# Optimization experiments

Measured on AMD Instinct MI355X. Metric: run time of the kernel, lower is better.

Reference implementation:

```python
import jax, jax.numpy as jnp
import numpy as np

N_NODES = 50000
N_EDGES = 600000
D_IN = 128
H = 128
D_OUT = 1


def setup_inputs() -> dict:
    key = jax.random.key(0)
    ks = jax.random.split(key, 6)
    x = jax.random.normal(ks[0], (N_NODES, D_IN), dtype=jnp.float32)
    edge_index = jax.random.randint(ks[1], (2, N_EDGES), 0, N_NODES, dtype=jnp.int32)
    # Glorot-ish init for GCN weights
    W1 = jax.random.normal(ks[2], (D_IN, H), dtype=jnp.float32) / np.sqrt(D_IN)
    W2 = jax.random.normal(ks[3], (H, H), dtype=jnp.float32) / np.sqrt(H)
    W3 = jax.random.normal(ks[4], (H, D_OUT), dtype=jnp.float32) / np.sqrt(H)
    b1 = jnp.zeros((H,), jnp.float32)
    b2 = jnp.zeros((H,), jnp.float32)
    b3 = jnp.zeros((D_OUT,), jnp.float32)
    return {"x": x, "edge_index": edge_index, "W1": W1, "b1": b1,
            "W2": W2, "b2": b2, "W3": W3, "b3": b3}


def _gcn_layer(h, src, dst, norm, self_norm, W, b, n_nodes):
    # GCNConv: h' = D^{-1/2}(A+I)D^{-1/2} (h W) + b
    hw = h @ W                                        # [N, F_out]
    msg = hw[src] * norm[:, None]                     # [E, F_out] edge gather
    agg = jax.ops.segment_sum(msg, dst, num_segments=n_nodes)
    agg = agg + hw * self_norm[:, None]               # self-loop contribution
    return agg + b


def reference(x, edge_index, W1, b1, W2, b2, W3, b3):
    # NOTE: F.dropout treated as identity (deterministic eval reference).
    n = x.shape[0]
    src, dst = edge_index[0], edge_index[1]
    # symmetric normalization with self-loops (PyG gcn_norm, edge_weight=1)
    deg = jnp.zeros((n,), x.dtype).at[dst].add(1.0) + 1.0
    dis = jax.lax.rsqrt(deg)                          # deg^{-1/2}
    norm = dis[src] * dis[dst]                        # per-edge norm
    self_norm = dis * dis
    h = jax.nn.relu(_gcn_layer(x, src, dst, norm, self_norm, W1, b1, n))
    h = jax.nn.relu(_gcn_layer(h, src, dst, norm, self_norm, W2, b2, n))
    h = jax.nn.relu(_gcn_layer(h, src, dst, norm, self_norm, W3, b3, n))
    return h
```

## Files before the change

kernel.cpp:

```cpp
#include <hip/hip_runtime.h>
#include <hip/hip_fp16.h>


typedef _Float16 v8h __attribute__((ext_vector_type(8)));
typedef float v4f __attribute__((ext_vector_type(4)));

__global__ __launch_bounds__(256) void k_count_wcast(const int* __restrict__ dst,
                                                     int* __restrict__ cnt, int nE,
                                                     int BE,
                                                     const float* __restrict__ W1,
                                                     const float* __restrict__ W2,
                                                     __half* __restrict__ Wt1,
                                                     __half* __restrict__ Wt2) {
    int b = blockIdx.x;
    if (b < BE) {
        int e = b * 256 + threadIdx.x;
        if (e < nE) atomicAdd(&cnt[dst[e]], 1);
    } else {
        int i = (b - BE) * 256 + threadIdx.x;
        int k = i >> 7, c = i & 127;
        Wt1[c * 128 + k] = __float2half(W1[i]);
        Wt2[c * 128 + k] = __float2half(W2[i]);
    }
}

__global__ __launch_bounds__(256) void k_scan_blk(const int* __restrict__ cnt,
                                                  float* __restrict__ dis,
                                                  int* __restrict__ excl,
                                                  int* __restrict__ blk_sum, int nN) {
    __shared__ int sm[256];
    const int t = threadIdx.x;
    int i = blockIdx.x * 256 + t;
    int v = (i < nN) ? cnt[i] : 0;
    if (i < nN) dis[i] = rsqrtf((float)v + 1.0f);
    sm[t] = v;
    __syncthreads();
#pragma unroll
    for (int off = 1; off < 256; off <<= 1) {
        int x = (t >= off) ? sm[t - off] : 0;
        __syncthreads();
        sm[t] += x;
        __syncthreads();
    }
    if (i < nN) excl[i] = sm[t] - v;
    if (t == 255) blk_sum[blockIdx.x] = sm[255];
}

__global__ __launch_bounds__(256) void k_scan_top(int* __restrict__ blk_sum, int nB) {
    __shared__ int sm[256];
    const int t = threadIdx.x;
    int v = (t < nB) ? blk_sum[t] : 0;
    sm[t] = v;
    __syncthreads();
#pragma unroll
    for (int off = 1; off < 256; off <<= 1) {
        int x = (t >= off) ? sm[t - off] : 0;
        __syncthreads();
        sm[t] += x;
        __syncthreads();
    }
    if (t < nB) blk_sum[t] = sm[t] - v;
    if (t == 0) blk_sum[nB] = sm[255];
}

__global__ __launch_bounds__(256) void k_scan_add(const int* __restrict__ excl,
                                                  const int* __restrict__ blk_sum,
                                                  int* __restrict__ row_ptr,
                                                  int* __restrict__ cursor,
                                                  int nN, int nB) {
    int i = blockIdx.x * 256 + threadIdx.x;
    if (i < nN) {
        int v = excl[i] + blk_sum[i >> 8];
        row_ptr[i] = v;
        cursor[i] = v;
    }
    if (i == 0) row_ptr[nN] = blk_sum[nB];
}

__global__ __launch_bounds__(256) void k_bin(const int* __restrict__ src,
                                             const int* __restrict__ dst,
                                             int* __restrict__ cursor,
                                             int* __restrict__ src_csr, int nE) {
    int e = blockIdx.x * 256 + threadIdx.x;
    if (e >= nE) return;
    int s = src[e], d = dst[e];
    int pos = atomicAdd(&cursor[d], 1);
    src_csr[pos] = s;
}

__device__ __forceinline__ float4 gather_row(const float2* __restrict__ Hv,
                                             const int* __restrict__ row_ptr,
                                             const int* __restrict__ src_csr,
                                             int g, int f4) {
    int beg = row_ptr[g], end = row_ptr[g + 1];
    float2 r0 = Hv[(size_t)g * 32 + f4];
    float2 lo = __half22float2(*(__half2*)&r0.x);
    float2 hi = __half22float2(*(__half2*)&r0.y);
    float4 acc = make_float4(lo.x, lo.y, hi.x, hi.y);
    int e = beg;
    for (; e + 8 <= end; e += 8) {
        int s[8];
#pragma unroll
        for (int j = 0; j < 8; ++j) s[j] = src_csr[e + j];
        float2 r[8];
#pragma unroll
        for (int j = 0; j < 8; ++j) r[j] = Hv[(size_t)s[j] * 32 + f4];
#pragma unroll
        for (int j = 0; j < 8; ++j) {
            float2 l2 = __half22float2(*(__half2*)&r[j].x);
            float2 h2 = __half22float2(*(__half2*)&r[j].y);
            acc.x += l2.x; acc.y += l2.y; acc.z += h2.x; acc.w += h2.y;
        }
    }
    if (e + 4 <= end) {
        int s[4];
#pragma unroll
        for (int j = 0; j < 4; ++j) s[j] = src_csr[e + j];
        float2 r[4];
#pragma unroll
        for (int j = 0; j < 4; ++j) r[j] = Hv[(size_t)s[j] * 32 + f4];
#pragma unroll
        for (int j = 0; j < 4; ++j) {
            float2 l2 = __half22float2(*(__half2*)&r[j].x);
            float2 h2 = __half22float2(*(__half2*)&r[j].y);
            acc.x += l2.x; acc.y += l2.y; acc.z += h2.x; acc.w += h2.y;
        }
        e += 4;
    }
    for (; e < end; ++e) {
        float2 r = Hv[(size_t)src_csr[e] * 32 + f4];
        float2 l2 = __half22float2(*(__half2*)&r.x);
        float2 h2 = __half22float2(*(__half2*)&r.y);
        acc.x += l2.x; acc.y += l2.y; acc.z += h2.x; acc.w += h2.y;
    }
    return acc;
}

__global__ __launch_bounds__(256) void k_gemm_mfma(const float* __restrict__ X32,
                                                   const __half* __restrict__ Wt,
                                                   const float* __restrict__ dis,
                                                   __half* __restrict__ HWS,
                                                   int nrows) {
    __shared__ __half xs[64 * 136];
    const int t = threadIdx.x;
    const int row0 = blockIdx.x * 64;

#pragma unroll
    for (int i = 0; i < 8; ++i) {
        int f = t + i * 256;
        int r = f >> 5, k4 = f & 31;
        int gr = row0 + r;
        float4 v = make_float4(0.f, 0.f, 0.f, 0.f);
        if (gr < nrows) v = ((const float4*)X32)[(size_t)gr * 32 + k4];
        __half2 h01 = __float22half2_rn(make_float2(v.x, v.y));
        __half2 h23 = __float22half2_rn(make_float2(v.z, v.w));
        float2 packed;
        *(__half2*)&packed.x = h01;
        *(__half2*)&packed.y = h23;
        *(float2*)&xs[r * 136 + k4 * 4] = packed;
    }
    __syncthreads();

    const int w = t >> 6;
    const int l = t & 63;
    const int mrow = l & 15;
    const int kq = l >> 4;

    v8h a[4];
#pragma unroll
    for (int kk = 0; kk < 4; ++kk)
        a[kk] = *(const v8h*)&xs[(w * 16 + mrow) * 136 + kk * 32 + kq * 8];

    v4f acc[8];
#pragma unroll
    for (int c = 0; c < 8; ++c) acc[c] = (v4f){0.f, 0.f, 0.f, 0.f};

#pragma unroll
    for (int kk = 0; kk < 4; ++kk) {
#pragma unroll
        for (int c = 0; c < 8; ++c) {
            v8h b = *(const v8h*)&Wt[(size_t)(c * 16 + mrow) * 128 + kk * 32 + kq * 8];
            acc[c] = __builtin_amdgcn_mfma_f32_16x16x32_f16(a[kk], b, acc[c], 0, 0, 0);
        }
    }

    float dn[4];
#pragma unroll
    for (int r = 0; r < 4; ++r) {
        int grow = row0 + w * 16 + kq * 4 + r;
        dn[r] = (grow < nrows) ? dis[grow] : 0.f;
    }
#pragma unroll
    for (int c = 0; c < 8; ++c) {
#pragma unroll
        for (int r = 0; r < 4; ++r) {
            int grow = row0 + w * 16 + kq * 4 + r;
            if (grow < nrows)
                HWS[(size_t)grow * 128 + c * 16 + mrow] =
                    __float2half(acc[c][r] * dn[r]);
        }
    }
}

__global__ __launch_bounds__(512) void k_gather_gemm(const __half* __restrict__ HWS1,
                                                     const int* __restrict__ row_ptr,
                                                     const int* __restrict__ src_csr,
                                                     const float* __restrict__ dis,
                                                     const float* __restrict__ bias,
                                                     const __half* __restrict__ Wt,
                                                     __half* __restrict__ HWS2,
                                                     int nN) {
    __shared__ __half xs[64 * 136];
    const int t = threadIdx.x;
    const int row0 = blockIdx.x * 64;
    const int hw_id = t >> 5;
    const int f4 = t & 31;
    const float2* Hv = (const float2*)HWS1;
    const float4 bv = ((const float4*)bias)[f4];

#pragma unroll 1
    for (int i = 0; i < 4; ++i) {
        int lr = i * 16 + hw_id;
        int g = row0 + lr;
        float4 h = make_float4(0.f, 0.f, 0.f, 0.f);
        if (g < nN) {
            float4 acc = gather_row(Hv, row_ptr, src_csr, g, f4);
            float dn = dis[g];
            h.x = fmaxf(acc.x * dn + bv.x, 0.f);
            h.y = fmaxf(acc.y * dn + bv.y, 0.f);
            h.z = fmaxf(acc.z * dn + bv.z, 0.f);
            h.w = fmaxf(acc.w * dn + bv.w, 0.f);
        }
        __half2 h01 = __float22half2_rn(make_float2(h.x, h.y));
        __half2 h23 = __float22half2_rn(make_float2(h.z, h.w));
        float2 packed;
        *(__half2*)&packed.x = h01;
        *(__half2*)&packed.y = h23;
        *(float2*)&xs[lr * 136 + f4 * 4] = packed;
    }
    __syncthreads();

    const int w = t >> 6;
    const int l = t & 63;
    const int mrow = l & 15;
    const int kq = l >> 4;
    const int rgrp = (w & 3) * 16;
    const int cgrp = (w >> 2) * 4;

    v8h a[4];
#pragma unroll
    for (int kk = 0; kk < 4; ++kk)
        a[kk] = *(const v8h*)&xs[(rgrp + mrow) * 136 + kk * 32 + kq * 8];

    v4f acc[4];
#pragma unroll
    for (int c = 0; c < 4; ++c) acc[c] = (v4f){0.f, 0.f, 0.f, 0.f};

#pragma unroll
    for (int kk = 0; kk < 4; ++kk) {
#pragma unroll
        for (int c = 0; c < 4; ++c) {
            v8h b = *(const v8h*)&Wt[(size_t)((cgrp + c) * 16 + mrow) * 128 + kk * 32 + kq * 8];
            acc[c] = __builtin_amdgcn_mfma_f32_16x16x32_f16(a[kk], b, acc[c], 0, 0, 0);
        }
    }

    float dn4[4];
#pragma unroll
    for (int r = 0; r < 4; ++r) {
        int grow = row0 + rgrp + kq * 4 + r;
        dn4[r] = (grow < nN) ? dis[grow] : 0.f;
    }
#pragma unroll
    for (int c = 0; c < 4; ++c) {
#pragma unroll
        for (int r = 0; r < 4; ++r) {
            int grow = row0 + rgrp + kq * 4 + r;
            if (grow < nN)
                HWS2[(size_t)grow * 128 + (cgrp + c) * 16 + mrow] =
                    __float2half(acc[c][r] * dn4[r]);
        }
    }
}

__global__ __launch_bounds__(256) void k_gather_gemv(const __half* __restrict__ HWS2,
                                                     const int* __restrict__ row_ptr,
                                                     const int* __restrict__ src_csr,
                                                     const float* __restrict__ dis,
                                                     const float* __restrict__ bias,
                                                     const float* __restrict__ W3,
                                                     float* __restrict__ hw3s, int nN) {
    int g = blockIdx.x * 8 + (threadIdx.x >> 5);
    if (g >= nN) return;
    int f4 = threadIdx.x & 31;
    float4 acc = gather_row((const float2*)HWS2, row_ptr, src_csr, g, f4);
    float dn = dis[g];
    float4 bv = ((const float4*)bias)[f4];
    float4 w  = ((const float4*)W3)[f4];
    float sum = fmaxf(acc.x * dn + bv.x, 0.f) * w.x
              + fmaxf(acc.y * dn + bv.y, 0.f) * w.y
              + fmaxf(acc.z * dn + bv.z, 0.f) * w.z
              + fmaxf(acc.w * dn + bv.w, 0.f) * w.w;
#pragma unroll
    for (int off = 16; off > 0; off >>= 1) sum += __shfl_down(sum, off, 32);
    if (f4 == 0) hw3s[g] = sum * dn;
}

__global__ __launch_bounds__(256) void k_gather3(const float* __restrict__ hw3s,
                                                 const int* __restrict__ row_ptr,
                                                 const int* __restrict__ src_csr,
                                                 const float* __restrict__ dis,
                                                 const float* __restrict__ b3,
                                                 float* __restrict__ out, int nN) {
    int i = blockIdx.x * 256 + threadIdx.x;
    if (i >= nN) return;
    float acc = hw3s[i];
    int beg = row_ptr[i], end = row_ptr[i + 1];
    for (int e = beg; e < end; ++e) acc += hw3s[src_csr[e]];
    out[i] = fmaxf(acc * dis[i] + b3[0], 0.f);
}

extern "C" void kernel_launch(void* const* d_in, const int* in_sizes, int n_in,
                              void* d_out, int out_size, void* d_ws, size_t ws_size,
                              hipStream_t stream) {
    const float* x  = (const float*)d_in[0];
    const int*   ei = (const int*)d_in[1];
    const float* W1 = (const float*)d_in[2];
    const float* b1 = (const float*)d_in[3];
    const float* W2 = (const float*)d_in[4];
    const float* b2 = (const float*)d_in[5];
    const float* W3 = (const float*)d_in[6];
    const float* b3 = (const float*)d_in[7];

    const int nN = in_sizes[0] / 128;
    const int nE = in_sizes[1] / 2;
    const int* src = ei;
    const int* dst = ei + nE;

    const int nB = (nN + 255) / 256;

    char* p = (char*)d_ws;
    int*    cnt      = (int*)p;           p += (size_t)nN * 4;
    int*    cursor   = (int*)p;           p += (size_t)nN * 4;
    int*    excl     = (int*)p;           p += (size_t)nN * 4;
    int*    blk_sum  = (int*)p;           p += (size_t)(nB + 1) * 4;
    int*    row_ptr  = (int*)p;           p += (size_t)(nN + 1) * 4;
    int*    src_csr  = (int*)p;           p += (size_t)nE * 4;
    float*  dis      = (float*)p;         p += (size_t)nN * 4;
    float*  hw3s     = (float*)p;         p += (size_t)nN * 4;
    p = (char*)(((uintptr_t)p + 255) & ~(uintptr_t)255);
    __half* Wt1      = (__half*)p;        p += (size_t)128 * 128 * 2;
    __half* Wt2      = (__half*)p;        p += (size_t)128 * 128 * 2;
    __half* bufA     = (__half*)p;        p += (size_t)nN * 128 * 2;
    p = (char*)(((uintptr_t)p + 255) & ~(uintptr_t)255);
    __half* bufB     = (__half*)p;        p += (size_t)nN * 128 * 2;

    const int BE  = (nE + 255) / 256;
    const int BN  = (nN + 255) / 256;
    const int BG  = (nN + 63) / 64;
    const int BGA = (nN + 7) / 8;

    hipMemsetAsync(cnt, 0, (size_t)nN * sizeof(int), stream);
    k_count_wcast<<<BE + 64, 256, 0, stream>>>(dst, cnt, nE, BE, W1, W2, Wt1, Wt2);
    k_scan_blk<<<nB, 256, 0, stream>>>(cnt, dis, excl, blk_sum, nN);
    k_scan_top<<<1, 256, 0, stream>>>(blk_sum, nB);
    k_scan_add<<<nB, 256, 0, stream>>>(excl, blk_sum, row_ptr, cursor, nN, nB);
    k_bin     <<<BE, 256, 0, stream>>>(src, dst, cursor, src_csr, nE);

    k_gemm_mfma<<<BG, 256, 0, stream>>>(x, Wt1, dis, bufA, nN);

    k_gather_gemm<<<BG, 512, 0, stream>>>(bufA, row_ptr, src_csr, dis, b1, Wt2,
                                          bufB, nN);

    k_gather_gemv<<<BGA, 256, 0, stream>>>(bufB, row_ptr, src_csr, dis, b2, W3,
                                           hw3s, nN);

    k_gather3<<<BN, 256, 0, stream>>>(hw3s, row_ptr, src_csr, dis, b3,
                                      (float*)d_out, nN);
}
```

Baseline: 248.0 us.

## Fuse scan top into scan add, dynamically schedule gather rows, prefetch weight fragments

Result: slower. 261.8 us (+5.6%).

```diff
diff --git a/kernel.cpp b/kernel.cpp
--- a/kernel.cpp
+++ b/kernel.cpp
@@ -46,7 +46,11 @@
     if (t == 255) blk_sum[blockIdx.x] = sm[255];
 }
 
-__global__ __launch_bounds__(256) void k_scan_top(int* __restrict__ blk_sum, int nB) {
+__global__ __launch_bounds__(256) void k_scan_add(const int* __restrict__ excl,
+                                                  const int* __restrict__ blk_sum,
+                                                  int* __restrict__ row_ptr,
+                                                  int* __restrict__ cursor,
+                                                  int nN, int nB) {
     __shared__ int sm[256];
     const int t = threadIdx.x;
     int v = (t < nB) ? blk_sum[t] : 0;
@@ -59,22 +63,15 @@
         sm[t] += x;
         __syncthreads();
     }
-    if (t < nB) blk_sum[t] = sm[t] - v;
-    if (t == 0) blk_sum[nB] = sm[255];
-}
-
-__global__ __launch_bounds__(256) void k_scan_add(const int* __restrict__ excl,
-                                                  const int* __restrict__ blk_sum,
-                                                  int* __restrict__ row_ptr,
-                                                  int* __restrict__ cursor,
-                                                  int nN, int nB) {
-    int i = blockIdx.x * 256 + threadIdx.x;
+    int i = blockIdx.x * 256 + t;
     if (i < nN) {
-        int v = excl[i] + blk_sum[i >> 8];
-        row_ptr[i] = v;
-        cursor[i] = v;
-    }
-    if (i == 0) row_ptr[nN] = blk_sum[nB];
+        int b = i >> 8;
+        int off = sm[b] - blk_sum[b];
+        int val = excl[i] + off;
+        row_ptr[i] = val;
+        cursor[i] = val;
+    }
+    if (i == 0) row_ptr[nN] = sm[255];
 }
 
 __global__ __launch_bounds__(256) void k_bin(const int* __restrict__ src,
@@ -211,16 +208,37 @@
                                                      __half* __restrict__ HWS2,
                                                      int nN) {
     __shared__ __half xs[64 * 136];
+    __shared__ int q;
     const int t = threadIdx.x;
     const int row0 = blockIdx.x * 64;
-    const int hw_id = t >> 5;
     const int f4 = t & 31;
     const float2* Hv = (const float2*)HWS1;
     const float4 bv = ((const float4*)bias)[f4];
 
-#pragma unroll 1
-    for (int i = 0; i < 4; ++i) {
-        int lr = i * 16 + hw_id;
+    const int w = t >> 6;
+    const int l = t & 63;
+    const int mrow = l & 15;
+    const int kq = l >> 4;
+    const int rgrp = (w & 3) * 16;
+    const int cgrp = (w >> 2) * 4;
+
+    if (t == 0) q = 0;
+
+    v8h bfrag[4][4];
+#pragma unroll
+    for (int kk = 0; kk < 4; ++kk)
+#pragma unroll
+        for (int c = 0; c < 4; ++c)
+            bfrag[kk][c] = *(const v8h*)&Wt[(size_t)((cgrp + c) * 16 + mrow) * 128
+                                            + kk * 32 + kq * 8];
+    __syncthreads();
+
+    const int bcast_lane = (l >> 5) << 5;
+    for (;;) {
+        int lr = 0;
+        if (f4 == 0) lr = atomicAdd(&q, 1);
+        lr = __shfl(lr, bcast_lane, 64);
+        if (lr >= 64) break;
         int g = row0 + lr;
         float4 h = make_float4(0.f, 0.f, 0.f, 0.f);
         if (g < nN) {
@@ -240,13 +258,6 @@
     }
     __syncthreads();
 
-    const int w = t >> 6;
-    const int l = t & 63;
-    const int mrow = l & 15;
-    const int kq = l >> 4;
-    const int rgrp = (w & 3) * 16;
-    const int cgrp = (w >> 2) * 4;
-
     v8h a[4];
 #pragma unroll
     for (int kk = 0; kk < 4; ++kk)
@@ -257,13 +268,11 @@
     for (int c = 0; c < 4; ++c) acc[c] = (v4f){0.f, 0.f, 0.f, 0.f};
 
 #pragma unroll
-    for (int kk = 0; kk < 4; ++kk) {
-#pragma unroll
-        for (int c = 0; c < 4; ++c) {
-            v8h b = *(const v8h*)&Wt[(size_t)((cgrp + c) * 16 + mrow) * 128 + kk * 32 + kq * 8];
-            acc[c] = __builtin_amdgcn_mfma_f32_16x16x32_f16(a[kk], b, acc[c], 0, 0, 0);
-        }
-    }
+    for (int kk = 0; kk < 4; ++kk)
+#pragma unroll
+        for (int c = 0; c < 4; ++c)
+            acc[c] = __builtin_amdgcn_mfma_f32_16x16x32_f16(a[kk], bfrag[kk][c],
+                                                            acc[c], 0, 0, 0);
 
     float dn4[4];
 #pragma unroll
@@ -363,7 +372,6 @@
     hipMemsetAsync(cnt, 0, (size_t)nN * sizeof(int), stream);
     k_count_wcast<<<BE + 64, 256, 0, stream>>>(dst, cnt, nE, BE, W1, W2, Wt1, Wt2);
     k_scan_blk<<<nB, 256, 0, stream>>>(cnt, dis, excl, blk_sum, nN);
-    k_scan_top<<<1, 256, 0, stream>>>(blk_sum, nB);
     k_scan_add<<<nB, 256, 0, stream>>>(excl, blk_sum, row_ptr, cursor, nN, nB);
     k_bin     <<<BE, 256, 0, stream>>>(src, dst, cursor, src_csr, nE);
 
```

## Fuse top-level scan into scan_add and merge edge binning into layer-1 GEMM

Applied to the files above, without the earlier changes.

After: 235.1 us. 5.2% less time.

```diff
diff --git a/kernel.cpp b/kernel.cpp
--- a/kernel.cpp
+++ b/kernel.cpp
@@ -46,7 +46,11 @@
     if (t == 255) blk_sum[blockIdx.x] = sm[255];
 }
 
-__global__ __launch_bounds__(256) void k_scan_top(int* __restrict__ blk_sum, int nB) {
+__global__ __launch_bounds__(256) void k_scan_add(const int* __restrict__ excl,
+                                                  const int* __restrict__ blk_sum,
+                                                  int* __restrict__ row_ptr,
+                                                  int* __restrict__ cursor,
+                                                  int nN, int nB) {
     __shared__ int sm[256];
     const int t = threadIdx.x;
     int v = (t < nB) ? blk_sum[t] : 0;
@@ -59,33 +63,15 @@
         sm[t] += x;
         __syncthreads();
     }
-    if (t < nB) blk_sum[t] = sm[t] - v;
-    if (t == 0) blk_sum[nB] = sm[255];
-}
-
-__global__ __launch_bounds__(256) void k_scan_add(const int* __restrict__ excl,
-                                                  const int* __restrict__ blk_sum,
-                                                  int* __restrict__ row_ptr,
-                                                  int* __restrict__ cursor,
-                                                  int nN, int nB) {
-    int i = blockIdx.x * 256 + threadIdx.x;
+    int i = blockIdx.x * 256 + t;
     if (i < nN) {
-        int v = excl[i] + blk_sum[i >> 8];
-        row_ptr[i] = v;
-        cursor[i] = v;
-    }
-    if (i == 0) row_ptr[nN] = blk_sum[nB];
-}
-
-__global__ __launch_bounds__(256) void k_bin(const int* __restrict__ src,
-                                             const int* __restrict__ dst,
-                                             int* __restrict__ cursor,
-                                             int* __restrict__ src_csr, int nE) {
-    int e = blockIdx.x * 256 + threadIdx.x;
-    if (e >= nE) return;
-    int s = src[e], d = dst[e];
-    int pos = atomicAdd(&cursor[d], 1);
-    src_csr[pos] = s;
+        int b = i >> 8;
+        int off = sm[b] - blk_sum[b];
+        int val = excl[i] + off;
+        row_ptr[i] = val;
+        cursor[i] = val;
+    }
+    if (i == 0) row_ptr[nN] = sm[255];
 }
 
 __device__ __forceinline__ float4 gather_row(const float2* __restrict__ Hv,
@@ -136,12 +122,26 @@
     return acc;
 }
 
-__global__ __launch_bounds__(256) void k_gemm_mfma(const float* __restrict__ X32,
-                                                   const __half* __restrict__ Wt,
-                                                   const float* __restrict__ dis,
-                                                   __half* __restrict__ HWS,
-                                                   int nrows) {
+__global__ __launch_bounds__(256) void k_gemm_bin(const float* __restrict__ X32,
+                                                  const __half* __restrict__ Wt,
+                                                  const float* __restrict__ dis,
+                                                  __half* __restrict__ HWS,
+                                                  int nrows, int BG,
+                                                  const int* __restrict__ src,
+                                                  const int* __restrict__ dst,
+                                                  int* __restrict__ cursor,
+                                                  int* __restrict__ src_csr, int nE) {
     __shared__ __half xs[64 * 136];
+    if (blockIdx.x >= BG) {
+        int e = (blockIdx.x - BG) * 256 + threadIdx.x;
+        if (e < nE) {
+            int s = src[e], d = dst[e];
+            int pos = atomicAdd(&cursor[d], 1);
+            src_csr[pos] = s;
+        }
+        return;
+    }
+
     const int t = threadIdx.x;
     const int row0 = blockIdx.x * 64;
 
@@ -363,11 +363,10 @@
     hipMemsetAsync(cnt, 0, (size_t)nN * sizeof(int), stream);
     k_count_wcast<<<BE + 64, 256, 0, stream>>>(dst, cnt, nE, BE, W1, W2, Wt1, Wt2);
     k_scan_blk<<<nB, 256, 0, stream>>>(cnt, dis, excl, blk_sum, nN);
-    k_scan_top<<<1, 256, 0, stream>>>(blk_sum, nB);
     k_scan_add<<<nB, 256, 0, stream>>>(excl, blk_sum, row_ptr, cursor, nN, nB);
-    k_bin     <<<BE, 256, 0, stream>>>(src, dst, cursor, src_csr, nE);
-
-    k_gemm_mfma<<<BG, 256, 0, stream>>>(x, Wt1, dis, bufA, nN);
+
+    k_gemm_bin<<<BG + BE, 256, 0, stream>>>(x, Wt1, dis, bufA, nN, BG,
+                                            src, dst, cursor, src_csr, nE);
 
     k_gather_gemm<<<BG, 512, 0, stream>>>(bufA, row_ptr, src_csr, dis, b1, Wt2,
                                           bufB, nN);
```
